# Kernel tuning notes

Measured on AMD Instinct MI355X. Metric: run time of the kernel, lower is better.

## Reference

```python
import jax, jax.numpy as jnp
import numpy as np

B, CIN, COUT, HID, H, W, K, PAD = 16, 64, 64, 32, 32, 32, 5, 2


def self_attention(x, Wq, Wk, Wv):
    # x: [B,C,H,W]; Wq,Wk: [HID,C]; Wv: [C,C]  (1x1 convs as channel matmuls)
    b, c, h, w = x.shape
    n = h * w
    xf = x.reshape(b, c, n)                      # [B,C,N]
    q = jnp.einsum('dc,bcn->bdn', Wq, xf)        # [B,HID,N]
    k = jnp.einsum('dc,bcn->bdn', Wk, xf)        # [B,HID,N]
    v = jnp.einsum('ec,bcn->ben', Wv, xf)        # [B,C,N]
    scores = jnp.einsum('bdn,bdm->bnm', q, k)    # [B,N,N]
    attn = jax.nn.softmax(scores, axis=-1)
    out = jnp.einsum('bcm,bnm->bcn', v, attn)    # aggregate values
    out = out.reshape(b, c, h, w)
    return x + out, attn                          # residual


def conv_lstm_cell(x, h, c, W_lstm, b_lstm):
    combined = jnp.concatenate([x, h], axis=1)   # [B,CIN+COUT,H,W]
    gates = jax.lax.conv_general_dilated(
        combined, W_lstm, window_strides=(1, 1),
        padding=[(PAD, PAD), (PAD, PAD)],
        dimension_numbers=('NCHW', 'OIHW', 'NCHW'))
    gates = gates + b_lstm[None, :, None, None]
    i, f, o, g = jnp.split(gates, 4, axis=1)
    i, f, o = jax.nn.sigmoid(i), jax.nn.sigmoid(f), jax.nn.sigmoid(o)
    g = jnp.tanh(g)
    c_new = f * c + i * g
    h_new = o * jnp.tanh(c_new)
    return h_new, c_new


def setup_inputs() -> dict:
    key = jax.random.key(0)
    ks = jax.random.split(key, 12)
    s = 0.05
    return {
        'x': jax.random.normal(ks[0], (B, CIN, H, W), jnp.float32),
        'h': jax.random.normal(ks[1], (B, COUT, H, W), jnp.float32),
        'c': jax.random.normal(ks[2], (B, COUT, H, W), jnp.float32),
        'Wq_x': jax.random.normal(ks[3], (HID, CIN), jnp.float32) * s,
        'Wk_x': jax.random.normal(ks[4], (HID, CIN), jnp.float32) * s,
        'Wv_x': jax.random.normal(ks[5], (CIN, CIN), jnp.float32) * s,
        'Wq_h': jax.random.normal(ks[6], (HID, COUT), jnp.float32) * s,
        'Wk_h': jax.random.normal(ks[7], (HID, COUT), jnp.float32) * s,
        'Wv_h': jax.random.normal(ks[8], (COUT, COUT), jnp.float32) * s,
        'W_lstm': jax.random.normal(ks[9], (4 * COUT, CIN + COUT, K, K), jnp.float32) * s,
        'b_lstm': jnp.zeros((4 * COUT,), jnp.float32),
    }


def reference(x, h, c, Wq_x, Wk_x, Wv_x, Wq_h, Wk_h, Wv_h, W_lstm, b_lstm):
    X, _ = self_attention(x, Wq_x, Wk_x, Wv_x)
    new_h, new_c = conv_lstm_cell(X, h, c, W_lstm, b_lstm)
    new_h, atten = self_attention(new_h, Wq_h, Wk_h, Wv_h)
    new_h = new_h + new_h  # faithful to `new_h += new_h`
    return new_h, new_c, atten
```

## Files before the change

### kernel.cpp

```cpp
#include <hip/hip_runtime.h>
#include <hip/hip_bf16.h>
#include <cstddef>
#include <cstdint>

#define NTOK 1024
#define NB   16
#define NC   64
#define NHID 32

#define PAD_BSTRIDE 165888
#define PAD_KSTRIDE 82944
#define PAD_BYTES   5308416

typedef __attribute__((ext_vector_type(8))) short short8;
typedef __attribute__((ext_vector_type(4))) float f32x4;

__device__ __forceinline__ ushort f2b(float f) {
  uint32_t u = __builtin_bit_cast(uint32_t, f);
  return (ushort)((u + 0x7FFFu + ((u >> 16) & 1u)) >> 16);
}
__device__ __forceinline__ float b2f(ushort u) {
  return __builtin_bit_cast(float, (uint32_t)u << 16);
}
__device__ __forceinline__ short8 ldw8(const float* __restrict__ p) {
  float4 f0 = *(const float4*)p, f1 = *(const float4*)(p + 4);
  short8 r;
  r[0] = (short)f2b(f0.x); r[1] = (short)f2b(f0.y);
  r[2] = (short)f2b(f0.z); r[3] = (short)f2b(f0.w);
  r[4] = (short)f2b(f1.x); r[5] = (short)f2b(f1.y);
  r[6] = (short)f2b(f1.z); r[7] = (short)f2b(f1.w);
  return r;
}
__device__ __forceinline__ float sigm(float x) { return 1.f / (1.f + __expf(-x)); }
__device__ __forceinline__ float tanh_fast(float x) {
  float e = __expf(2.f * x);
  return 1.f - 2.f / (e + 1.f);
}

__global__ __launch_bounds__(256) void tpose_pad_kernel(
    const float* __restrict__ src, ushort* __restrict__ dst) {
  __shared__ float tile[64][65];
  int t = threadIdx.x;
  int n0 = blockIdx.x * 64, b = blockIdx.y;
  const float* s = src + (size_t)b * NC * NTOK;
#pragma unroll
  for (int r = 0; r < 4; ++r) {
    int c = r * 16 + (t >> 4);
    int nl = (t & 15) * 4;
    float4 v = *(const float4*)(s + (size_t)c * NTOK + n0 + nl);
    tile[c][nl] = v.x; tile[c][nl + 1] = v.y; tile[c][nl + 2] = v.z; tile[c][nl + 3] = v.w;
  }
  __syncthreads();
  int tok = t >> 2, c0 = (t & 3) * 16;
  __attribute__((aligned(16))) ushort tmp[16];
#pragma unroll
  for (int i = 0; i < 16; ++i) tmp[i] = f2b(tile[c0 + i][tok]);
  int gtok = n0 + tok;
  ushort* d = dst + (size_t)b * PAD_BSTRIDE +
              ((gtok >> 5) + 2) * 2304 + ((gtok & 31) + 2) * 64 + c0;
  *(uint4*)(d)     = *(const uint4*)(tmp);
  *(uint4*)(d + 8) = *(const uint4*)(tmp + 8);
}

__global__ __launch_bounds__(256) void qkvproj_kernel(
    const float* __restrict__ x, const float* __restrict__ Wq,
    const float* __restrict__ Wk, const float* __restrict__ Wv,
    ushort* __restrict__ qT, ushort* __restrict__ kT, ushort* __restrict__ vb) {
  __shared__ float tile[64][65];
  __shared__ ushort xb[64][72];
  __shared__ ushort sq[64][32], sk[64][32];
  int t = threadIdx.x, wave = t >> 6, lane = t & 63;
  int lo = lane & 15, lg = lane >> 4;
  int n0 = blockIdx.x * 64, b = blockIdx.y;
  const float* s = x + (size_t)b * NC * NTOK;
#pragma unroll
  for (int r = 0; r < 4; ++r) {
    int c = r * 16 + (t >> 4);
    int nl = (t & 15) * 4;
    float4 v = *(const float4*)(s + (size_t)c * NTOK + n0 + nl);
    tile[c][nl] = v.x; tile[c][nl + 1] = v.y; tile[c][nl + 2] = v.z; tile[c][nl + 3] = v.w;
  }
  __syncthreads();
  {
    int tok = t >> 2, c0 = (t & 3) * 16;
    __attribute__((aligned(16))) ushort tmp[16];
#pragma unroll
    for (int i = 0; i < 16; ++i) tmp[i] = f2b(tile[c0 + i][tok]);
    *(uint4*)(&xb[tok][c0])     = *(const uint4*)(tmp);
    *(uint4*)(&xb[tok][c0 + 8]) = *(const uint4*)(tmp + 8);
  }
  __syncthreads();
  const ushort* xrow = &xb[wave * 16 + lo][8 * lg];
  short8 a0 = *(const short8*)(xrow);
  short8 a1 = *(const short8*)(xrow + 32);
  f32x4 aq[2], ak[2];
#pragma unroll
  for (int dg = 0; dg < 2; ++dg) {
    short8 wq0 = ldw8(Wq + (size_t)(dg * 16 + lo) * NC + 8 * lg);
    short8 wq1 = ldw8(Wq + (size_t)(dg * 16 + lo) * NC + 32 + 8 * lg);
    short8 wk0 = ldw8(Wk + (size_t)(dg * 16 + lo) * NC + 8 * lg);
    short8 wk1 = ldw8(Wk + (size_t)(dg * 16 + lo) * NC + 32 + 8 * lg);
    f32x4 z = {0.f, 0.f, 0.f, 0.f};
    aq[dg] = __builtin_amdgcn_mfma_f32_16x16x32_bf16(a0, wq0, z, 0, 0, 0);
    aq[dg] = __builtin_amdgcn_mfma_f32_16x16x32_bf16(a1, wq1, aq[dg], 0, 0, 0);
    ak[dg] = __builtin_amdgcn_mfma_f32_16x16x32_bf16(a0, wk0, z, 0, 0, 0);
    ak[dg] = __builtin_amdgcn_mfma_f32_16x16x32_bf16(a1, wk1, ak[dg], 0, 0, 0);
  }
  f32x4 av[4];
#pragma unroll
  for (int g = 0; g < 4; ++g) {
    short8 wv0 = ldw8(Wv + (size_t)(g * 16 + lo) * NC + 8 * lg);
    short8 wv1 = ldw8(Wv + (size_t)(g * 16 + lo) * NC + 32 + 8 * lg);
    f32x4 z = {0.f, 0.f, 0.f, 0.f};
    av[g] = __builtin_amdgcn_mfma_f32_16x16x32_bf16(wv0, a0, z, 0, 0, 0);
    av[g] = __builtin_amdgcn_mfma_f32_16x16x32_bf16(wv1, a1, av[g], 0, 0, 0);
  }
#pragma unroll
  for (int dg = 0; dg < 2; ++dg)
#pragma unroll
    for (int r = 0; r < 4; ++r) {
      sq[wave * 16 + 4 * lg + r][dg * 16 + lo] = f2b(aq[dg][r]);
      sk[wave * 16 + 4 * lg + r][dg * 16 + lo] = f2b(ak[dg][r]);
    }
  ushort* vbase = vb + (size_t)b * NC * NTOK + n0 + wave * 16 + lo;
#pragma unroll
  for (int g = 0; g < 4; ++g)
#pragma unroll
    for (int r = 0; r < 4; ++r)
      vbase[(size_t)(g * 16 + lg * 4 + r) * NTOK] = f2b(av[g][r]);
  __syncthreads();
  int tok = t >> 2, d0 = (t & 3) * 8;
  size_t base = ((size_t)b * NTOK + n0 + tok) * NHID + d0;
  *(short8*)(qT + base) = *(const short8*)(&sq[tok][d0]);
  *(short8*)(kT + base) = *(const short8*)(&sk[tok][d0]);
}

#define SP 1048
template <bool ATTN2>
__global__ __launch_bounds__(256) void attn_fused_kernel(
    const ushort* __restrict__ qT, const ushort* __restrict__ kT,
    const ushort* __restrict__ vb, const float* __restrict__ resid,
    float* __restrict__ attnf, float* __restrict__ outf,
    ushort* __restrict__ outb_pad, float scale) {
  __shared__ ushort s_lds[16 * SP];
  __shared__ float wmax[4][16], wsum[4][16];
  int t = threadIdx.x, wave = t >> 6, lane = t & 63;
  int lo = lane & 15, lg = lane >> 4;
  int n0 = blockIdx.x * 16, b = blockIdx.y;
  int m0 = wave * 256;
  short8 a = *(const short8*)(qT + ((size_t)b * NTOK + n0 + lo) * NHID + 8 * lg);
  f32x4 acc[16];
#pragma unroll
  for (int j = 0; j < 16; ++j) {
    short8 bf = *(const short8*)(kT + ((size_t)b * NTOK + m0 + j * 16 + lo) * NHID + 8 * lg);
    f32x4 z = {0.f, 0.f, 0.f, 0.f};
    acc[j] = __builtin_amdgcn_mfma_f32_16x16x32_bf16(a, bf, z, 0, 0, 0);
  }
  float pm[4];
#pragma unroll
  for (int r = 0; r < 4; ++r) {
    float m = acc[0][r];
#pragma unroll
    for (int j = 1; j < 16; ++j) m = fmaxf(m, acc[j][r]);
#pragma unroll
    for (int off = 1; off < 16; off <<= 1) m = fmaxf(m, __shfl_xor(m, off, 64));
    pm[r] = m;
  }
  if (lo == 0)
#pragma unroll
    for (int r = 0; r < 4; ++r) wmax[wave][4 * lg + r] = pm[r];
  __syncthreads();
  float mr[4];
#pragma unroll
  for (int r = 0; r < 4; ++r)
    mr[r] = fmaxf(fmaxf(wmax[0][4 * lg + r], wmax[1][4 * lg + r]),
                  fmaxf(wmax[2][4 * lg + r], wmax[3][4 * lg + r]));
  float ps[4] = {0.f, 0.f, 0.f, 0.f};
#pragma unroll
  for (int j = 0; j < 16; ++j)
#pragma unroll
    for (int r = 0; r < 4; ++r) {
      float e = __expf(acc[j][r] - mr[r]);
      acc[j][r] = e;
      ps[r] += e;
    }
#pragma unroll
  for (int r = 0; r < 4; ++r)
#pragma unroll
    for (int off = 1; off < 16; off <<= 1) ps[r] += __shfl_xor(ps[r], off, 64);
  if (lo == 0)
#pragma unroll
    for (int r = 0; r < 4; ++r) wsum[wave][4 * lg + r] = ps[r];
  __syncthreads();
  float inv[4];
#pragma unroll
  for (int r = 0; r < 4; ++r)
    inv[r] = 1.f / (wsum[0][4 * lg + r] + wsum[1][4 * lg + r] +
                    wsum[2][4 * lg + r] + wsum[3][4 * lg + r]);
#pragma unroll
  for (int j = 0; j < 16; ++j)
#pragma unroll
    for (int r = 0; r < 4; ++r)
      s_lds[(4 * lg + r) * SP + m0 + j * 16 + lo] = f2b(acc[j][r] * inv[r]);
  __syncthreads();
  if constexpr (ATTN2) {
    int ml = lane * 4;
    float* abase = attnf + ((size_t)b * NTOK + n0) * NTOK + m0;
#pragma unroll
    for (int n = 0; n < 16; ++n) {
      ushort4 sv = *(const ushort4*)(s_lds + n * SP + m0 + ml);
      float4 o;
      o.x = b2f(sv.x); o.y = b2f(sv.y); o.z = b2f(sv.z); o.w = b2f(sv.w);
      *(float4*)(abase + (size_t)n * NTOK + ml) = o;
    }
  }
  int cb = wave * 16;
  const ushort* vbb = vb + ((size_t)b * NC + cb + lo) * NTOK;
  f32x4 acc2 = {0.f, 0.f, 0.f, 0.f}, acc3 = {0.f, 0.f, 0.f, 0.f};
  for (int ms = 0; ms < NTOK; ms += 64) {
    short8 af0 = *(const short8*)(s_lds + lo * SP + ms + 8 * lg);
    short8 bf0 = *(const short8*)(vbb + ms + 8 * lg);
    short8 af1 = *(const short8*)(s_lds + lo * SP + ms + 32 + 8 * lg);
    short8 bf1 = *(const short8*)(vbb + ms + 32 + 8 * lg);
    acc2 = __builtin_amdgcn_mfma_f32_16x16x32_bf16(af0, bf0, acc2, 0, 0, 0);
    acc3 = __builtin_amdgcn_mfma_f32_16x16x32_bf16(af1, bf1, acc3, 0, 0, 0);
  }
#pragma unroll
  for (int r = 0; r < 4; ++r) acc2[r] += acc3[r];
  int c = cb + lo;
  float4 rv = *(const float4*)(resid + ((size_t)b * NC + c) * NTOK + n0 + 4 * lg);
  float rvv[4] = {rv.x, rv.y, rv.z, rv.w};
  if constexpr (ATTN2) {
    float4 o;
    o.x = scale * (rvv[0] + acc2[0]); o.y = scale * (rvv[1] + acc2[1]);
    o.z = scale * (rvv[2] + acc2[2]); o.w = scale * (rvv[3] + acc2[3]);
    *(float4*)(outf + ((size_t)b * NC + c) * NTOK + n0 + 4 * lg) = o;
  } else {
#pragma unroll
    for (int r = 0; r < 4; ++r) {
      int tok = n0 + 4 * lg + r;
      float val = scale * (rvv[r] + acc2[r]);
      outb_pad[(size_t)b * PAD_BSTRIDE + ((tok >> 5) + 2) * 2304 +
               ((tok & 31) + 2) * 64 + c] = f2b(val);
    }
  }
}

__global__ __launch_bounds__(256) void wpre_kernel(
    const float* __restrict__ W, ushort* __restrict__ Wb) {
  int idx = blockIdx.x * 256 + threadIdx.x;
  const float* src = W + (size_t)idx * 25;
#pragma unroll
  for (int kk = 0; kk < 25; ++kk)
    Wb[((size_t)(idx >> 7) * 25 + kk) * 128 + (idx & 127)] = f2b(src[kk]);
}

#define AP 76
#define BP 76
__global__ __launch_bounds__(256, 2) void conv_lstm_kernel(
    const ushort* __restrict__ pad,
    const ushort* __restrict__ Wb,
    const float* __restrict__ bias, const float* __restrict__ c_in,
    float* __restrict__ c_out, float* __restrict__ h_out) {
  __shared__ ushort ldsA[2][128 * AP];
  __shared__ ushort ldsB[216 * BP];
  int t = threadIdx.x;
  int lane = t & 63, lo = lane & 15, lg = lane >> 4;
  int wid = t >> 6, cb = wid & 1, ph = wid >> 1;
  int pt = blockIdx.x, chh = blockIdx.y, b = blockIdx.z;
  const ushort* pb = pad + (size_t)b * PAD_BSTRIDE + (size_t)(pt * 2) * 2304;

  for (int i = t; i < 1728; i += 256) {
    int pxw = i >> 3, ch8 = (i & 7) * 8;
    uint4 v = *(const uint4*)(pb + (size_t)pxw * 64 + ch8);
    *(uint4*)(ldsB + pxw * BP + ch8) = v;
  }

  const ushort *wsrc0, *wsrc1, *wsrc2, *wsrc3;
  int adst0, adst1, adst2, adst3;
  {
    int i0 = t, i1 = 256 + t, i2 = 512 + t, i3 = 768 + t;
    int r0 = i0 >> 3, r1 = i1 >> 3, r2 = i2 >> 3, r3 = i3 >> 3;
    wsrc0 = Wb + (size_t)((r0 >> 5) * 64 + chh * 32 + (r0 & 31)) * 3200 + (i0 & 7) * 8;
    wsrc1 = Wb + (size_t)((r1 >> 5) * 64 + chh * 32 + (r1 & 31)) * 3200 + (i1 & 7) * 8;
    wsrc2 = Wb + (size_t)((r2 >> 5) * 64 + chh * 32 + (r2 & 31)) * 3200 + (i2 & 7) * 8;
    wsrc3 = Wb + (size_t)((r3 >> 5) * 64 + chh * 32 + (r3 & 31)) * 3200 + (i3 & 7) * 8;
    adst0 = r0 * AP + (i0 & 7) * 8;
    adst1 = r1 * AP + (i1 & 7) * 8;
    adst2 = r2 * AP + (i2 & 7) * 8;
    adst3 = r3 * AP + (i3 & 7) * 8;
  }
  uint4 w0 = *(const uint4*)(wsrc0);
  uint4 w1 = *(const uint4*)(wsrc1);
  uint4 w2 = *(const uint4*)(wsrc2);
  uint4 w3 = *(const uint4*)(wsrc3);

  f32x4 acc[4][2];
#pragma unroll
  for (int i = 0; i < 4; ++i)
#pragma unroll
    for (int j = 0; j < 2; ++j) acc[i][j] = {0.f, 0.f, 0.f, 0.f};

  __syncthreads();
  *(uint4*)(&ldsA[0][adst0]) = w0;
  *(uint4*)(&ldsA[0][adst1]) = w1;
  *(uint4*)(&ldsA[0][adst2]) = w2;
  *(uint4*)(&ldsA[0][adst3]) = w3;
  w0 = *(const uint4*)(wsrc0 + 128);
  w1 = *(const uint4*)(wsrc1 + 128);
  w2 = *(const uint4*)(wsrc2 + 128);
  w3 = *(const uint4*)(wsrc3 + 128);
  __syncthreads();

  for (int s = 0; s < 50; ++s) {
    int cur = s & 1;
    if (s < 49) {
      int nxt = cur ^ 1;
      *(uint4*)(&ldsA[nxt][adst0]) = w0;
      *(uint4*)(&ldsA[nxt][adst1]) = w1;
      *(uint4*)(&ldsA[nxt][adst2]) = w2;
      *(uint4*)(&ldsA[nxt][adst3]) = w3;
      int s2 = (s < 48) ? s + 2 : 49;
      int koff = (s2 < 25) ? s2 * 128 : (s2 - 25) * 128 + 64;
      w0 = *(const uint4*)(wsrc0 + koff);
      w1 = *(const uint4*)(wsrc1 + koff);
      w2 = *(const uint4*)(wsrc2 + koff);
      w3 = *(const uint4*)(wsrc3 + koff);
    }
    int kh = (s >= 25);
    int tap = s - kh * 25;
    int ky = tap / 5, kx = tap - 5 * ky;
    int bbase = (ky * 36 + kx) * BP;
#pragma unroll
    for (int icc = 0; icc < 2; ++icc) {
      short8 af[4], bf[2];
#pragma unroll
      for (int i = 0; i < 4; ++i)
        af[i] = *(const short8*)(&ldsA[cur][(i * 32 + cb * 16 + lo) * AP + icc * 32 + 8 * lg]);
#pragma unroll
      for (int j = 0; j < 2; ++j)
        bf[j] = *(const short8*)(ldsB + bbase + (ph * 36 + j * 16 + lo) * BP + icc * 32 + 8 * lg);
#pragma unroll
      for (int i = 0; i < 4; ++i)
#pragma unroll
        for (int j = 0; j < 2; ++j)
          acc[i][j] = __builtin_amdgcn_mfma_f32_16x16x32_bf16(af[i], bf[j], acc[i][j], 0, 0, 0);
    }
    __syncthreads();
    if (s == 24) {
      for (int i = t; i < 1728; i += 256) {
        int pxw = i >> 3, ch8 = (i & 7) * 8;
        uint4 v = *(const uint4*)(pb + PAD_KSTRIDE + (size_t)pxw * 64 + ch8);
        *(uint4*)(ldsB + pxw * BP + ch8) = v;
      }
      __syncthreads();
    }
  }

#pragma unroll
  for (int j = 0; j < 2; ++j)
#pragma unroll
    for (int r = 0; r < 4; ++r) {
      int ch = chh * 32 + cb * 16 + lg * 4 + r;
      int p = pt * 64 + ph * 32 + j * 16 + lo;
      size_t ci = ((size_t)b * NC + ch) * NTOK + p;
      float iv = sigm(acc[0][j][r] + bias[ch]);
      float fv = sigm(acc[1][j][r] + bias[64 + ch]);
      float ov = sigm(acc[2][j][r] + bias[128 + ch]);
      float gv = tanh_fast(acc[3][j][r] + bias[192 + ch]);
      float cn = fv * c_in[ci] + iv * gv;
      c_out[ci] = cn;
      h_out[ci] = ov * tanh_fast(cn);
    }
}

extern "C" void kernel_launch(void* const* d_in, const int* in_sizes, int n_in,
                              void* d_out, int out_size, void* d_ws, size_t ws_size,
                              hipStream_t stream) {
  const float* x      = (const float*)d_in[0];
  const float* h      = (const float*)d_in[1];
  const float* c      = (const float*)d_in[2];
  const float* Wq_x   = (const float*)d_in[3];
  const float* Wk_x   = (const float*)d_in[4];
  const float* Wv_x   = (const float*)d_in[5];
  const float* Wq_h   = (const float*)d_in[6];
  const float* Wk_h   = (const float*)d_in[7];
  const float* Wv_h   = (const float*)d_in[8];
  const float* W_lstm = (const float*)d_in[9];
  const float* b_lstm = (const float*)d_in[10];

  float* out   = (float*)d_out;
  float* new_h = out;
  float* new_c = out + 1048576;
  float* atten = out + 2097152;

  ushort* wsu = (ushort*)d_ws;
  ushort* qT  = wsu;
  ushort* kT  = wsu + 524288;
  ushort* vb  = wsu + 1048576;

  ushort* Wb    = (ushort*)(atten + 8388608);
  ushort* pad   = (ushort*)(atten + 9437184);
  float*  h_mid = new_h;

  dim3 blk(256);
  hipMemsetAsync(pad, 0, PAD_BYTES, stream);
  qkvproj_kernel<<<dim3(16, NB), blk, 0, stream>>>(x, Wq_x, Wk_x, Wv_x, qT, kT, vb);
  attn_fused_kernel<false><<<dim3(64, NB), blk, 0, stream>>>(
      qT, kT, vb, x, nullptr, nullptr, pad , 1.0f);
  wpre_kernel<<<128, blk, 0, stream>>>(W_lstm, Wb);
  tpose_pad_kernel<<<dim3(16, NB), blk, 0, stream>>>(h, pad + PAD_KSTRIDE);
  conv_lstm_kernel<<<dim3(16, 2, NB), blk, 0, stream>>>(pad, Wb, b_lstm, c, new_c, h_mid);
  qkvproj_kernel<<<dim3(16, NB), blk, 0, stream>>>(h_mid, Wq_h, Wk_h, Wv_h, qT, kT, vb);
  attn_fused_kernel<true><<<dim3(64, NB), blk, 0, stream>>>(
      qT, kT, vb, h_mid, atten, new_h, nullptr, 2.0f);
}
```

Baseline: 127.7 us.

## Load conv weights straight to registers, stage both input halves in LDS

The conv-LSTM kernel stops staging weight tiles through a double-buffered LDS array. Each wave now loads its MFMA weight fragments directly from global memory into registers, using a three-deep rotating prefetch. Both channel halves of the padded input are loaded into a larger LDS buffer up front, which removes the per-step barrier and the mid-loop reload. The attention-probability output writes become nontemporal stores. The trade-off is higher register pressure and redundant global weight reads across waves, plus a larger LDS footprint that may limit occupancy.

Measured after the change: 184.8 us. 44.7% more time.

```diff
diff --git a/kernel.cpp b/kernel.cpp
--- a/kernel.cpp
+++ b/kernel.cpp
@@ -209,9 +209,8 @@
 #pragma unroll
     for (int n = 0; n < 16; ++n) {
       ushort4 sv = *(const ushort4*)(s_lds + n * SP + m0 + ml);
-      float4 o;
-      o.x = b2f(sv.x); o.y = b2f(sv.y); o.z = b2f(sv.z); o.w = b2f(sv.w);
-      *(float4*)(abase + (size_t)n * NTOK + ml) = o;
+      f32x4 o = {b2f(sv.x), b2f(sv.y), b2f(sv.z), b2f(sv.w)};
+      __builtin_nontemporal_store(o, (f32x4*)(abase + (size_t)n * NTOK + ml));
     }
   }
   int cb = wave * 16;
@@ -255,45 +254,67 @@
     Wb[((size_t)(idx >> 7) * 25 + kk) * 128 + (idx & 127)] = f2b(src[kk]);
 }
 
-#define AP 76
 #define BP 76
 __global__ __launch_bounds__(256, 2) void conv_lstm_kernel(
     const ushort* __restrict__ pad,
     const ushort* __restrict__ Wb,
     const float* __restrict__ bias, const float* __restrict__ c_in,
     float* __restrict__ c_out, float* __restrict__ h_out) {
-  __shared__ ushort ldsA[2][128 * AP];
-  __shared__ ushort ldsB[216 * BP];
+  __shared__ ushort ldsB[432 * BP];
   int t = threadIdx.x;
   int lane = t & 63, lo = lane & 15, lg = lane >> 4;
   int wid = t >> 6, cb = wid & 1, ph = wid >> 1;
   int pt = blockIdx.x, chh = blockIdx.y, b = blockIdx.z;
   const ushort* pb = pad + (size_t)b * PAD_BSTRIDE + (size_t)(pt * 2) * 2304;
 
-  for (int i = t; i < 1728; i += 256) {
+  for (int i = t; i < 3456; i += 256) {
     int pxw = i >> 3, ch8 = (i & 7) * 8;
-    uint4 v = *(const uint4*)(pb + (size_t)pxw * 64 + ch8);
+    int kh = pxw >= 216, w = pxw - kh * 216;
+    uint4 v = *(const uint4*)(pb + (size_t)kh * PAD_KSTRIDE + (size_t)w * 64 + ch8);
     *(uint4*)(ldsB + pxw * BP + ch8) = v;
   }
 
-  const ushort *wsrc0, *wsrc1, *wsrc2, *wsrc3;
-  int adst0, adst1, adst2, adst3;
-  {
-    int i0 = t, i1 = 256 + t, i2 = 512 + t, i3 = 768 + t;
-    int r0 = i0 >> 3, r1 = i1 >> 3, r2 = i2 >> 3, r3 = i3 >> 3;
-    wsrc0 = Wb + (size_t)((r0 >> 5) * 64 + chh * 32 + (r0 & 31)) * 3200 + (i0 & 7) * 8;
-    wsrc1 = Wb + (size_t)((r1 >> 5) * 64 + chh * 32 + (r1 & 31)) * 3200 + (i1 & 7) * 8;
-    wsrc2 = Wb + (size_t)((r2 >> 5) * 64 + chh * 32 + (r2 & 31)) * 3200 + (i2 & 7) * 8;
-    wsrc3 = Wb + (size_t)((r3 >> 5) * 64 + chh * 32 + (r3 & 31)) * 3200 + (i3 & 7) * 8;
-    adst0 = r0 * AP + (i0 & 7) * 8;
-    adst1 = r1 * AP + (i1 & 7) * 8;
-    adst2 = r2 * AP + (i2 & 7) * 8;
-    adst3 = r3 * AP + (i3 & 7) * 8;
-  }
-  uint4 w0 = *(const uint4*)(wsrc0);
-  uint4 w1 = *(const uint4*)(wsrc1);
-  uint4 w2 = *(const uint4*)(wsrc2);
-  uint4 w3 = *(const uint4*)(wsrc3);
+  const ushort* wbase0 = Wb + (size_t)(0 * 64 + chh * 32 + cb * 16 + lo) * 3200 + 8 * lg;
+  const ushort* wbase1 = Wb + (size_t)(1 * 64 + chh * 32 + cb * 16 + lo) * 3200 + 8 * lg;
+  const ushort* wbase2 = Wb + (size_t)(2 * 64 + chh * 32 + cb * 16 + lo) * 3200 + 8 * lg;
+  const ushort* wbase3 = Wb + (size_t)(3 * 64 + chh * 32 + cb * 16 + lo) * 3200 + 8 * lg;
+
+#define KOFF(sv) (((sv) < 25) ? (sv) * 128 : ((sv) - 25) * 128 + 64)
+#define LOADA(dst, sv)                                                         \
+  {                                                                            \
+    int _s = (sv) <= 49 ? (sv) : 49;                                           \
+    int _k = KOFF(_s);                                                         \
+    dst[0] = *(const short8*)(wbase0 + _k);                                    \
+    dst[1] = *(const short8*)(wbase0 + _k + 32);                               \
+    dst[2] = *(const short8*)(wbase1 + _k);                                    \
+    dst[3] = *(const short8*)(wbase1 + _k + 32);                               \
+    dst[4] = *(const short8*)(wbase2 + _k);                                    \
+    dst[5] = *(const short8*)(wbase2 + _k + 32);                               \
+    dst[6] = *(const short8*)(wbase3 + _k);                                    \
+    dst[7] = *(const short8*)(wbase3 + _k + 32);                               \
+  }
+#define STEP(wreg, sv)                                                         \
+  {                                                                            \
+    int _kh = (sv) >= 25;                                                      \
+    int _tap = (sv) - _kh * 25;                                                \
+    int _ky = _tap / 5, _kx = _tap - 5 * _ky;                                  \
+    int _bb = (_kh * 216 + _ky * 36 + _kx) * BP;                               \
+    _Pragma("unroll") for (int icc = 0; icc < 2; ++icc) {                      \
+      short8 bf[2];                                                            \
+      _Pragma("unroll") for (int j = 0; j < 2; ++j)                            \
+        bf[j] = *(const short8*)(ldsB + _bb +                                  \
+                 (ph * 36 + j * 16 + lo) * BP + icc * 32 + 8 * lg);            \
+      _Pragma("unroll") for (int i = 0; i < 4; ++i)                            \
+        _Pragma("unroll") for (int j = 0; j < 2; ++j)                          \
+          acc[i][j] = __builtin_amdgcn_mfma_f32_16x16x32_bf16(                 \
+              wreg[i * 2 + icc], bf[j], acc[i][j], 0, 0, 0);                   \
+    }                                                                          \
+  }
+
+  short8 w0[8], w1[8], w2[8];
+  LOADA(w0, 0);
+  LOADA(w1, 1);
+  LOADA(w2, 2);
 
   f32x4 acc[4][2];
 #pragma unroll
@@ -302,60 +323,17 @@
     for (int j = 0; j < 2; ++j) acc[i][j] = {0.f, 0.f, 0.f, 0.f};
 
   __syncthreads();
-  *(uint4*)(&ldsA[0][adst0]) = w0;
-  *(uint4*)(&ldsA[0][adst1]) = w1;
-  *(uint4*)(&ldsA[0][adst2]) = w2;
-  *(uint4*)(&ldsA[0][adst3]) = w3;
-  w0 = *(const uint4*)(wsrc0 + 128);
-  w1 = *(const uint4*)(wsrc1 + 128);
-  w2 = *(const uint4*)(wsrc2 + 128);
-  w3 = *(const uint4*)(wsrc3 + 128);
-  __syncthreads();
-
-  for (int s = 0; s < 50; ++s) {
-    int cur = s & 1;
-    if (s < 49) {
-      int nxt = cur ^ 1;
-      *(uint4*)(&ldsA[nxt][adst0]) = w0;
-      *(uint4*)(&ldsA[nxt][adst1]) = w1;
-      *(uint4*)(&ldsA[nxt][adst2]) = w2;
-      *(uint4*)(&ldsA[nxt][adst3]) = w3;
-      int s2 = (s < 48) ? s + 2 : 49;
-      int koff = (s2 < 25) ? s2 * 128 : (s2 - 25) * 128 + 64;
-      w0 = *(const uint4*)(wsrc0 + koff);
-      w1 = *(const uint4*)(wsrc1 + koff);
-      w2 = *(const uint4*)(wsrc2 + koff);
-      w3 = *(const uint4*)(wsrc3 + koff);
-    }
-    int kh = (s >= 25);
-    int tap = s - kh * 25;
-    int ky = tap / 5, kx = tap - 5 * ky;
-    int bbase = (ky * 36 + kx) * BP;
-#pragma unroll
-    for (int icc = 0; icc < 2; ++icc) {
-      short8 af[4], bf[2];
-#pragma unroll
-      for (int i = 0; i < 4; ++i)
-        af[i] = *(const short8*)(&ldsA[cur][(i * 32 + cb * 16 + lo) * AP + icc * 32 + 8 * lg]);
-#pragma unroll
-      for (int j = 0; j < 2; ++j)
-        bf[j] = *(const short8*)(ldsB + bbase + (ph * 36 + j * 16 + lo) * BP + icc * 32 + 8 * lg);
-#pragma unroll
-      for (int i = 0; i < 4; ++i)
-#pragma unroll
-        for (int j = 0; j < 2; ++j)
-          acc[i][j] = __builtin_amdgcn_mfma_f32_16x16x32_bf16(af[i], bf[j], acc[i][j], 0, 0, 0);
-    }
-    __syncthreads();
-    if (s == 24) {
-      for (int i = t; i < 1728; i += 256) {
-        int pxw = i >> 3, ch8 = (i & 7) * 8;
-        uint4 v = *(const uint4*)(pb + PAD_KSTRIDE + (size_t)pxw * 64 + ch8);
-        *(uint4*)(ldsB + pxw * BP + ch8) = v;
-      }
-      __syncthreads();
-    }
-  }
+
+  for (int st = 0; st < 48; st += 3) {
+    STEP(w0, st);     LOADA(w0, st + 3);
+    STEP(w1, st + 1); LOADA(w1, st + 4);
+    STEP(w2, st + 2); LOADA(w2, st + 5);
+  }
+  STEP(w0, 48);
+  STEP(w1, 49);
+#undef STEP
+#undef LOADA
+#undef KOFF
 
 #pragma unroll
   for (int j = 0; j < 2; ++j)
@@ -404,7 +382,7 @@
   float*  h_mid = new_h;
 
   dim3 blk(256);
-  hipMemsetAsync(pad, 0, PAD_BYTES, stream);
+  (void)hipMemsetAsync(pad, 0, PAD_BYTES, stream);
   qkvproj_kernel<<<dim3(16, NB), blk, 0, stream>>>(x, Wq_x, Wk_x, Wv_x, qT, kT, vb);
   attn_fused_kernel<false><<<dim3(64, NB), blk, 0, stream>>>(
       qT, kT, vb, x, nullptr, nullptr, pad , 1.0f);
```
